# Performance work log

Measured on AMD Instinct MI355X. Metric: run time of the kernel, lower is better.

## Reference

```python
import jax, jax.numpy as jnp
import numpy as np

D_MODEL = 1024; D_STATE = 128; EXPAND = 2; HEADDIM = 64
D_INNER = EXPAND * D_MODEL; NHEADS = D_INNER // HEADDIM; PF = 2  # param_factor for complex
BATCH = 2; SEQ = 2048
DT_MIN = 0.001; DT_MAX = 0.1


def setup_inputs() -> dict:
    key = jax.random.key(0)
    k = jax.random.split(key, 10)
    u = jax.random.normal(k[0], (BATCH, SEQ, D_MODEL), jnp.float32)
    in_proj_w = jax.random.normal(k[1], (2 * D_INNER, D_MODEL), jnp.float32) * (D_MODEL ** -0.5)
    dt_projs_weight = jax.random.normal(k[2], (NHEADS, D_INNER), jnp.float32) * 0.02
    dt_projs_bias = (jax.random.uniform(k[3], (NHEADS,), jnp.float32)
                     * (np.log(DT_MAX) - np.log(DT_MIN)) + np.log(DT_MIN)).astype(jnp.float32)
    x_proj_w = jax.random.normal(k[4], (NHEADS * (1 + 2 * D_STATE * PF), D_INNER), jnp.float32) * (D_INNER ** -0.5)
    A = jnp.stack([-jax.random.uniform(k[5], (NHEADS, D_STATE), dtype=jnp.float32),
                   jax.random.normal(k[6], (NHEADS, D_STATE), jnp.float32) * 0.1], axis=-1)  # (H,N,2)
    D = jnp.ones((NHEADS,), jnp.float32)
    norm_B_w = jnp.ones((2 * D_STATE,), jnp.float32)
    norm_C_w = jnp.ones((2 * D_STATE,), jnp.float32)
    out_proj_w = jax.random.normal(k[7], (D_MODEL, D_INNER), jnp.float32) * (D_INNER ** -0.5)
    return {"u": u, "in_proj_w": in_proj_w, "dt_projs_weight": dt_projs_weight,
            "dt_projs_bias": dt_projs_bias, "x_proj_w": x_proj_w, "A": A, "D": D,
            "norm_B_w": norm_B_w, "norm_C_w": norm_C_w, "out_proj_w": out_proj_w}


def _rms_norm(x, w, eps=1e-6):
    return x * jax.lax.rsqrt(jnp.mean(x * x, axis=-1, keepdims=True) + eps) * w


def reference(u, in_proj_w, dt_projs_weight, dt_projs_bias, x_proj_w, A, D,
              norm_B_w, norm_C_w, out_proj_w):
    Bsz, L, _ = u.shape
    xz = u @ in_proj_w.T                        # (B,L,2*d_inner)
    x, z = jnp.split(xz, 2, axis=-1)
    x = jax.nn.silu(x)                          # (B,L,d_inner)
    dt = jax.nn.softplus(x @ dt_projs_weight.T + dt_projs_bias)  # (B,L,H)

    BCp = (x @ x_proj_w.T).reshape(Bsz, L, NHEADS, -1)
    BC = BCp[..., :2 * D_STATE * PF].reshape(Bsz, L, NHEADS, 2, D_STATE, PF)
    Bn = _rms_norm(BC[..., 0, :, :].reshape(Bsz, L, NHEADS, D_STATE * PF), norm_B_w)
    Cn = _rms_norm(BC[..., 1, :, :].reshape(Bsz, L, NHEADS, D_STATE * PF), norm_C_w)
    Bn = Bn.reshape(Bsz, L, NHEADS, D_STATE, PF)
    Cn = Cn.reshape(Bsz, L, NHEADS, D_STATE, PF)
    Bc = jax.lax.complex(Bn[..., 0], Bn[..., 1])  # (B,L,H,N) complex64
    Cc = jax.lax.complex(Cn[..., 0], Cn[..., 1])
    Ac = jax.lax.complex(A[..., 0], A[..., 1])    # (H,N) complex64

    xh = x.reshape(Bsz, L, NHEADS, HEADDIM)
    x_sum = xh.sum(axis=-1)                       # (B,L,H) -- kernel sums x_t over headdim
    zt = Ac[None, None] * (0.5 * dt)[..., None]   # (B,L,H,N) complex: A*dt/2
    den = 1.0 - zt
    abar = (1.0 + zt) / den                       # bilinear (Tustin) discretization
    u_in = Bc * ((dt * x_sum)[..., None] / den)   # Bbar * sum(x_t)

    def step(h, inp):
        a, b = inp
        h = a * h + b
        return h, h

    h0 = jnp.zeros((Bsz, NHEADS, D_STATE), jnp.complex64)
    _, hs = jax.lax.scan(step, h0, (jnp.swapaxes(abar, 0, 1), jnp.swapaxes(u_in, 0, 1)))
    hs = jnp.swapaxes(hs, 0, 1)                   # (B,L,H,N)
    y_red = jnp.real(Cc * hs).sum(axis=-1)        # (B,L,H), Re(C*h) reduced over state
    y = (xh * (y_red + D)[..., None]).reshape(Bsz, L, D_INNER)
    y = y * jax.nn.silu(z)
    return y @ out_proj_w.T
```

## Files before the change

kernel.cpp:

```cpp
#include <hip/hip_runtime.h>

#define BATCH   2
#define SEQ     2048
#define DMODEL  1024
#define DINNER  2048
#define NHEADS  32
#define HEADDIM 64
#define DSTATE  128
#define BLTOT   (BATCH * SEQ)
#define NCHUNK  32
#define CHUNK   64

#define OFF_UB   0ull
#define OFF_WXZ  8388608ull
#define OFF_WBC  16777216ull
#define OFF_WOUT 83886080ull
#define OFF_XB   88080384ull
#define OFF_YB   104857600ull
#define OFF_BC   121634816ull
#define OFF_SZ   255852544ull
#define OFF_DT   272629760ull
#define OFF_XS   273154048ull
#define OFF_YR   273678336ull
#define OFF_CA   274202624ull
#define OFF_CS   276299776ull
#define OFF_HI   278396928ull

typedef __attribute__((ext_vector_type(8))) short bf16x8;
typedef __attribute__((ext_vector_type(4))) float f32x4;

__device__ __forceinline__ float b2f(unsigned short u) {
    return __uint_as_float(((unsigned)u) << 16);
}
__device__ __forceinline__ unsigned short f2b(float f) {
    unsigned x = __float_as_uint(f);
    unsigned r = (x + 0x7fffu + ((x >> 16) & 1u)) >> 16;
    return (unsigned short)r;
}
__device__ __forceinline__ float silu_f(float v) {
    return v / (1.0f + __expf(-v));
}
__device__ __forceinline__ float softplus_f(float v) {
    return (v > 20.0f) ? v : log1pf(__expf(v));
}

__device__ __forceinline__ void gload_lds16(const void* g, void* l) {
    __builtin_amdgcn_global_load_lds(
        (const __attribute__((address_space(1))) unsigned int*)g,
        (__attribute__((address_space(3))) unsigned int*)l, 16, 0, 0);
}

__global__ __launch_bounds__(256) void conv_all_kernel(
    const float* __restrict__ u, const float* __restrict__ ipw,
    const float* __restrict__ opw, const float* __restrict__ xpw,
    unsigned short* __restrict__ u_b, unsigned short* __restrict__ w_xz,
    unsigned short* __restrict__ w_out, unsigned short* __restrict__ w_bc) {
    long idx = (long)blockIdx.x * 256 + threadIdx.x;
    if (idx >= 2621440L) {
        long e = (idx - 2621440L) * 4;
        long c = e >> 11, k = e & 2047;
        const float* s = xpw + ((c >> 9) * 513 + (c & 511)) * 2048 + k;
        float4 v = *(const float4*)s;
        ushort4 o = {f2b(v.x), f2b(v.y), f2b(v.z), f2b(v.w)};
        *(ushort4*)&w_bc[e] = o;
        return;
    }
    const float* src;
    unsigned short* dst;
    long i;
    if (idx < 1048576L)      { src = u;   dst = u_b;   i = idx; }
    else if (idx < 2097152L) { src = ipw; dst = w_xz;  i = idx - 1048576L; }
    else                     { src = opw; dst = w_out; i = idx - 2097152L; }
    float4 v = *(const float4*)&src[i * 4];
    ushort4 o = {f2b(v.x), f2b(v.y), f2b(v.z), f2b(v.w)};
    *(ushort4*)&dst[i * 4] = o;
}

template <int K, int MODE>
__global__ __launch_bounds__(256) void gemm_mfma(
    const unsigned short* __restrict__ A, const unsigned short* __restrict__ B,
    void* __restrict__ C0, void* __restrict__ C1, float* __restrict__ C2,
    int N) {
    __shared__ short ldsA[128 * 32];
    __shared__ short ldsB[128 * 32];
    int tid = threadIdx.x;
    int row0 = blockIdx.y * 128, col0 = blockIdx.x * 128;
    int lane = tid & 63, wave = tid >> 6;
    int wrow = (wave >> 1) * 64, wcol = (wave & 1) * 64;
    int m = lane & 15, quad = lane >> 4;

    f32x4 acc[4][4];
#pragma unroll
    for (int i = 0; i < 4; ++i)
#pragma unroll
        for (int j = 0; j < 4; ++j) acc[i][j] = (f32x4){0.f, 0.f, 0.f, 0.f};

    int r = tid >> 2, c8 = (tid & 3) * 8;
    const unsigned short* Ag = A + (size_t)(row0 + r) * K + c8;
    const unsigned short* Bg = B + (size_t)(col0 + r) * K + c8;
    short* la = ldsA + tid * 8;
    short* lb = ldsB + tid * 8;

    for (int k0 = 0; k0 < K; k0 += 32) {
        gload_lds16(Ag + k0, la);
        gload_lds16(Ag + (size_t)64 * K + k0, la + 2048);
        gload_lds16(Bg + k0, lb);
        gload_lds16(Bg + (size_t)64 * K + k0, lb + 2048);
        __syncthreads();
        bf16x8 af[4], bfr[4];
#pragma unroll
        for (int i = 0; i < 4; ++i)
            af[i] = *(const bf16x8*)&ldsA[(wrow + i * 16 + m) * 32 + quad * 8];
#pragma unroll
        for (int j = 0; j < 4; ++j)
            bfr[j] = *(const bf16x8*)&ldsB[(wcol + j * 16 + m) * 32 + quad * 8];
#pragma unroll
        for (int i = 0; i < 4; ++i)
#pragma unroll
            for (int j = 0; j < 4; ++j)
                acc[i][j] = __builtin_amdgcn_mfma_f32_16x16x32_bf16(
                    af[i], bfr[j], acc[i][j], 0, 0, 0);
        __syncthreads();
    }

    if (MODE == 1) {
        bool isx = (col0 < DINNER);
        if (isx) {
            int head = (col0 + wcol) >> 6;
            float ssum[4][4];
#pragma unroll
            for (int i = 0; i < 4; ++i)
#pragma unroll
                for (int reg = 0; reg < 4; ++reg) ssum[i][reg] = 0.f;
#pragma unroll
            for (int i = 0; i < 4; ++i)
#pragma unroll
                for (int reg = 0; reg < 4; ++reg) {
                    int row = row0 + wrow + i * 16 + quad * 4 + reg;
#pragma unroll
                    for (int j = 0; j < 4; ++j) {
                        int col = col0 + wcol + j * 16 + m;
                        float s = silu_f(acc[i][j][reg]);
                        ((unsigned short*)C0)[(size_t)row * DINNER + col] = f2b(s);
                        ssum[i][reg] += s;
                    }
                }
#pragma unroll
            for (int i = 0; i < 4; ++i)
#pragma unroll
                for (int reg = 0; reg < 4; ++reg) {
                    float s = ssum[i][reg];
                    s += __shfl_xor(s, 1);
                    s += __shfl_xor(s, 2);
                    s += __shfl_xor(s, 4);
                    s += __shfl_xor(s, 8);
                    if (m == 0) {
                        int row = row0 + wrow + i * 16 + quad * 4 + reg;
                        C2[(size_t)row * NHEADS + head] = s;
                    }
                }
        } else {
#pragma unroll
            for (int i = 0; i < 4; ++i)
#pragma unroll
                for (int reg = 0; reg < 4; ++reg) {
                    int row = row0 + wrow + i * 16 + quad * 4 + reg;
#pragma unroll
                    for (int j = 0; j < 4; ++j) {
                        int col = col0 + wcol + j * 16 + m - DINNER;
                        float s = silu_f(acc[i][j][reg]);
                        ((unsigned short*)C1)[(size_t)row * DINNER + col] = f2b(s);
                    }
                }
        }
    } else {
#pragma unroll
        for (int i = 0; i < 4; ++i)
#pragma unroll
            for (int reg = 0; reg < 4; ++reg) {
                int row = row0 + wrow + i * 16 + quad * 4 + reg;
#pragma unroll
                for (int j = 0; j < 4; ++j) {
                    int col = col0 + wcol + j * 16 + m;
                    float v = acc[i][j][reg];
                    if (MODE == 0)
                        ((float*)C0)[(size_t)row * N + col] = v;
                    else
                        ((unsigned short*)C0)[(size_t)row * N + col] = f2b(v);
                }
            }
    }
}

__global__ __launch_bounds__(256) void dt_kernel(
    const unsigned short* __restrict__ x, const float* __restrict__ dtw,
    const float* __restrict__ dtb, float* __restrict__ dt) {
    __shared__ float xs[16][132];
    __shared__ float ws[32][132];
    int r0 = blockIdx.x * 16;
    int t = threadIdx.x;
    int lrow = t >> 4, lc8 = (t & 15) * 8;
    int lh = t >> 3, lc16 = (t & 7) * 16;
    int row = t >> 4, h0 = t & 15;
    float acc0 = 0.f, acc1 = 0.f;

    for (int kc = 0; kc < DINNER; kc += 128) {
        ushort4 a = *(const ushort4*)&x[(size_t)(r0 + lrow) * DINNER + kc + lc8];
        ushort4 b = *(const ushort4*)&x[(size_t)(r0 + lrow) * DINNER + kc + lc8 + 4];
        xs[lrow][lc8 + 0] = b2f(a.x); xs[lrow][lc8 + 1] = b2f(a.y);
        xs[lrow][lc8 + 2] = b2f(a.z); xs[lrow][lc8 + 3] = b2f(a.w);
        xs[lrow][lc8 + 4] = b2f(b.x); xs[lrow][lc8 + 5] = b2f(b.y);
        xs[lrow][lc8 + 6] = b2f(b.z); xs[lrow][lc8 + 7] = b2f(b.w);
#pragma unroll
        for (int q = 0; q < 4; ++q) {
            float4 w = *(const float4*)&dtw[(size_t)lh * DINNER + kc + lc16 + q * 4];
            *(float4*)&ws[lh][lc16 + q * 4] = w;
        }
        __syncthreads();
#pragma unroll
        for (int k = 0; k < 128; k += 4) {
            float4 xv = *(const float4*)&xs[row][k];
            float4 w0 = *(const float4*)&ws[h0][k];
            float4 w1 = *(const float4*)&ws[h0 + 16][k];
            acc0 += xv.x * w0.x + xv.y * w0.y + xv.z * w0.z + xv.w * w0.w;
            acc1 += xv.x * w1.x + xv.y * w1.y + xv.z * w1.z + xv.w * w1.w;
        }
        __syncthreads();
    }
    dt[(size_t)(r0 + row) * NHEADS + h0]      = softplus_f(acc0 + dtb[h0]);
    dt[(size_t)(r0 + row) * NHEADS + h0 + 16] = softplus_f(acc1 + dtb[h0 + 16]);
}

__device__ __forceinline__ void coefs(
    float ar, float ai, float dtv, float xsv, float Br, float Bi,
    float& abr, float& abi, float& ur, float& ui) {
    float hd = 0.5f * dtv;
    float ztr = ar * hd, zti = ai * hd;
    float denr = 1.0f - ztr;
    float s2 = 1.0f / (denr * denr + zti * zti);
    float invr = denr * s2, invi = zti * s2;
    float opr = 1.0f + ztr;
    abr = opr * invr - zti * invi;
    abi = opr * invi + zti * invr;
    float coef = dtv * xsv;
    float cr = coef * invr, ci = coef * invi;
    ur = Br * cr - Bi * ci;
    ui = Br * ci + Bi * cr;
}

__global__ __launch_bounds__(64) void scan_pass1(
    const unsigned short* __restrict__ bc, const float* __restrict__ dt,
    const float* __restrict__ xsum, const float* __restrict__ A,
    const float* __restrict__ wB, float2* __restrict__ cA,
    float2* __restrict__ cS) {
    int blk = blockIdx.x;
    int bh = blk >> 5, c = blk & (NCHUNK - 1);
    int b = bh >> 5, h = bh & 31;
    int t = threadIdx.x;
    float4 av = *(const float4*)&A[(h * DSTATE + 2 * t) * 2];
    float4 wv = *(const float4*)&wB[4 * t];
    int l0 = c * CHUNK;
    const unsigned short* base = bc + ((size_t)(b * SEQ + l0)) * 16384 + h * 512;
    const float* dtp = dt + (b * SEQ + l0) * NHEADS + h;
    const float* xsp = xsum + (b * SEQ + l0) * NHEADS + h;

    float pr0 = 1.f, pi0 = 0.f, sr0 = 0.f, si0 = 0.f;
    float pr1 = 1.f, pi1 = 0.f, sr1 = 0.f, si1 = 0.f;
    for (int l = 0; l < CHUNK; ++l) {
        uint2 bw = *(const uint2*)&base[(size_t)l * 16384 + 4 * t];
        float Br0 = b2f((unsigned short)(bw.x & 0xffff));
        float Bi0 = b2f((unsigned short)(bw.x >> 16));
        float Br1 = b2f((unsigned short)(bw.y & 0xffff));
        float Bi1 = b2f((unsigned short)(bw.y >> 16));
        float ss = Br0 * Br0 + Bi0 * Bi0 + Br1 * Br1 + Bi1 * Bi1;
#pragma unroll
        for (int off = 1; off < 64; off <<= 1) ss += __shfl_xor(ss, off);
        float scale = rsqrtf(ss * (1.0f / 256.0f) + 1e-6f);
        Br0 *= scale * wv.x; Bi0 *= scale * wv.y;
        Br1 *= scale * wv.z; Bi1 *= scale * wv.w;
        float dtv = dtp[l * NHEADS], xsv = xsp[l * NHEADS];
        float abr, abi, ur, ui;
        coefs(av.x, av.y, dtv, xsv, Br0, Bi0, abr, abi, ur, ui);
        float ns = abr * sr0 - abi * si0 + ur;
        float nsi = abr * si0 + abi * sr0 + ui;
        sr0 = ns; si0 = nsi;
        float np = abr * pr0 - abi * pi0;
        float npi = abr * pi0 + abi * pr0;
        pr0 = np; pi0 = npi;
        coefs(av.z, av.w, dtv, xsv, Br1, Bi1, abr, abi, ur, ui);
        ns = abr * sr1 - abi * si1 + ur;
        nsi = abr * si1 + abi * sr1 + ui;
        sr1 = ns; si1 = nsi;
        np = abr * pr1 - abi * pi1;
        npi = abr * pi1 + abi * pr1;
        pr1 = np; pi1 = npi;
    }
    size_t idx = ((size_t)bh * NCHUNK + c) * DSTATE + 2 * t;
    *(float4*)&cA[idx] = (float4){pr0, pi0, pr1, pi1};
    *(float4*)&cS[idx] = (float4){sr0, si0, sr1, si1};
}

__global__ __launch_bounds__(128) void scan_fixup(
    const float2* __restrict__ cA, const float2* __restrict__ cS,
    float2* __restrict__ hin) {
    int bh = blockIdx.x;
    int n = threadIdx.x;
    float hr = 0.f, hi = 0.f;
    for (int c = 0; c < NCHUNK; ++c) {
        size_t idx = ((size_t)bh * NCHUNK + c) * DSTATE + n;
        hin[idx] = {hr, hi};
        float2 a = cA[idx];
        float2 s = cS[idx];
        float nhr = a.x * hr - a.y * hi + s.x;
        float nhi = a.x * hi + a.y * hr + s.y;
        hr = nhr; hi = nhi;
    }
}

__global__ __launch_bounds__(64) void scan_pass2(
    const unsigned short* __restrict__ bc, const float* __restrict__ dt,
    const float* __restrict__ xsum, const float* __restrict__ A,
    const float* __restrict__ wB, const float* __restrict__ wC,
    const float2* __restrict__ hin, float* __restrict__ yredp) {
    int blk = blockIdx.x;
    int bh = blk >> 5, c = blk & (NCHUNK - 1);
    int b = bh >> 5, h = bh & 31;
    int t = threadIdx.x;
    float4 av = *(const float4*)&A[(h * DSTATE + 2 * t) * 2];
    float4 wbv = *(const float4*)&wB[4 * t];
    float4 wcv = *(const float4*)&wC[4 * t];
    int l0 = c * CHUNK;
    const unsigned short* base = bc + ((size_t)(b * SEQ + l0)) * 16384 + h * 512;
    const float* dtp = dt + (b * SEQ + l0) * NHEADS + h;
    const float* xsp = xsum + (b * SEQ + l0) * NHEADS + h;
    float* yp = yredp + (size_t)(b * SEQ + l0) * NHEADS + h;

    float4 h0v = *(const float4*)&hin[((size_t)bh * NCHUNK + c) * DSTATE + 2 * t];
    float hr0 = h0v.x, hi0 = h0v.y, hr1 = h0v.z, hi1 = h0v.w;

    for (int l = 0; l < CHUNK; ++l) {
        uint2 bw = *(const uint2*)&base[(size_t)l * 16384 + 4 * t];
        uint2 cw = *(const uint2*)&base[(size_t)l * 16384 + 256 + 4 * t];
        float Br0 = b2f((unsigned short)(bw.x & 0xffff));
        float Bi0 = b2f((unsigned short)(bw.x >> 16));
        float Br1 = b2f((unsigned short)(bw.y & 0xffff));
        float Bi1 = b2f((unsigned short)(bw.y >> 16));
        float Cr0 = b2f((unsigned short)(cw.x & 0xffff));
        float Ci0 = b2f((unsigned short)(cw.x >> 16));
        float Cr1 = b2f((unsigned short)(cw.y & 0xffff));
        float Ci1 = b2f((unsigned short)(cw.y >> 16));
        float ssB = Br0 * Br0 + Bi0 * Bi0 + Br1 * Br1 + Bi1 * Bi1;
        float ssC = Cr0 * Cr0 + Ci0 * Ci0 + Cr1 * Cr1 + Ci1 * Ci1;
#pragma unroll
        for (int off = 1; off < 64; off <<= 1) {
            ssB += __shfl_xor(ssB, off);
            ssC += __shfl_xor(ssC, off);
        }
        float sB = rsqrtf(ssB * (1.0f / 256.0f) + 1e-6f);
        float sC = rsqrtf(ssC * (1.0f / 256.0f) + 1e-6f);
        Br0 *= sB * wbv.x; Bi0 *= sB * wbv.y;
        Br1 *= sB * wbv.z; Bi1 *= sB * wbv.w;
        Cr0 *= sC * wcv.x; Ci0 *= sC * wcv.y;
        Cr1 *= sC * wcv.z; Ci1 *= sC * wcv.w;
        float dtv = dtp[l * NHEADS], xsv = xsp[l * NHEADS];
        float abr, abi, ur, ui;
        coefs(av.x, av.y, dtv, xsv, Br0, Bi0, abr, abi, ur, ui);
        float nhr = abr * hr0 - abi * hi0 + ur;
        float nhi = abr * hi0 + abi * hr0 + ui;
        hr0 = nhr; hi0 = nhi;
        coefs(av.z, av.w, dtv, xsv, Br1, Bi1, abr, abi, ur, ui);
        nhr = abr * hr1 - abi * hi1 + ur;
        nhi = abr * hi1 + abi * hr1 + ui;
        hr1 = nhr; hi1 = nhi;
        float y = Cr0 * hr0 - Ci0 * hi0 + Cr1 * hr1 - Ci1 * hi1;
#pragma unroll
        for (int off = 1; off < 64; off <<= 1) y += __shfl_xor(y, off);
        if (t == 0) yp[(size_t)l * NHEADS] = y;
    }
}

__global__ __launch_bounds__(256) void yfuse_kernel(
    const unsigned short* __restrict__ x, const unsigned short* __restrict__ sz,
    const float* __restrict__ yredp, const float* __restrict__ Dv,
    unsigned short* __restrict__ y) {
    int i = (blockIdx.x * 256 + threadIdx.x) * 4;
    int r = i >> 11;
    int k = i & (DINNER - 1);
    int h = k >> 6;
    float yr = yredp[(size_t)r * NHEADS + h] + Dv[h];
    ushort4 xv = *(const ushort4*)&x[i];
    ushort4 zv = *(const ushort4*)&sz[i];
    ushort4 o = {f2b(b2f(xv.x) * yr * b2f(zv.x)),
                 f2b(b2f(xv.y) * yr * b2f(zv.y)),
                 f2b(b2f(xv.z) * yr * b2f(zv.z)),
                 f2b(b2f(xv.w) * yr * b2f(zv.w))};
    *(ushort4*)&y[i] = o;
}

extern "C" void kernel_launch(void* const* d_in, const int* in_sizes, int n_in,
                              void* d_out, int out_size, void* d_ws, size_t ws_size,
                              hipStream_t stream) {
    const float* u   = (const float*)d_in[0];
    const float* ipw = (const float*)d_in[1];
    const float* dtw = (const float*)d_in[2];
    const float* dtb = (const float*)d_in[3];
    const float* xpw = (const float*)d_in[4];
    const float* A   = (const float*)d_in[5];
    const float* Dv  = (const float*)d_in[6];
    const float* wB  = (const float*)d_in[7];
    const float* wC  = (const float*)d_in[8];
    const float* opw = (const float*)d_in[9];
    float* out = (float*)d_out;
    char* ws = (char*)d_ws;

    unsigned short* u_b   = (unsigned short*)(ws + OFF_UB);
    unsigned short* w_xz  = (unsigned short*)(ws + OFF_WXZ);
    unsigned short* w_bc  = (unsigned short*)(ws + OFF_WBC);
    unsigned short* w_out = (unsigned short*)(ws + OFF_WOUT);
    unsigned short* x_b   = (unsigned short*)(ws + OFF_XB);
    unsigned short* y_b   = (unsigned short*)(ws + OFF_YB);
    unsigned short* bc    = (unsigned short*)(ws + OFF_BC);
    unsigned short* sz    = (unsigned short*)(ws + OFF_SZ);
    float* dt    = (float*)(ws + OFF_DT);
    float* xsum  = (float*)(ws + OFF_XS);
    float* yredp = (float*)(ws + OFF_YR);
    float2* cA   = (float2*)(ws + OFF_CA);
    float2* cS   = (float2*)(ws + OFF_CS);
    float2* hin  = (float2*)(ws + OFF_HI);

    conv_all_kernel<<<43008, 256, 0, stream>>>(u, ipw, opw, xpw,
                                               u_b, w_xz, w_out, w_bc);

    gemm_mfma<1024, 1><<<dim3(32, 32), 256, 0, stream>>>(
        u_b, w_xz, x_b, sz, xsum, 4096);
    dt_kernel<<<BLTOT / 16, 256, 0, stream>>>(x_b, dtw, dtb, dt);
    gemm_mfma<2048, 2><<<dim3(128, 32), 256, 0, stream>>>(
        x_b, w_bc, bc, nullptr, nullptr, 16384);

    scan_pass1<<<BATCH * NHEADS * NCHUNK, 64, 0, stream>>>(
        bc, dt, xsum, A, wB, cA, cS);
    scan_fixup<<<BATCH * NHEADS, 128, 0, stream>>>(cA, cS, hin);
    scan_pass2<<<BATCH * NHEADS * NCHUNK, 64, 0, stream>>>(
        bc, dt, xsum, A, wB, wC, hin, yredp);

    yfuse_kernel<<<BLTOT * DINNER / 4 / 256, 256, 0, stream>>>(
        x_b, sz, yredp, Dv, y_b);
    gemm_mfma<2048, 0><<<dim3(8, 32), 256, 0, stream>>>(
        y_b, w_out, out, nullptr, nullptr, 1024);
}
```

Baseline: 837.5 us.

## Fuse RMS sum-of-squares into BC GEMM epilogue and split-K the out projection

The BC projection GEMM epilogue now accumulates per-row, per-(head,B/C) sums of squares via shuffles and atomics into a small buffer. The scan passes read these instead of doing wave-wide shuffle reductions every timestep. The output GEMM is split four ways along K with atomicAdd into a pre-zeroed output, giving 1024 blocks instead of 256 to fill the GPU. This adds two memsets and float atomics, so output summation order becomes nondeterministic. The norms are now taken from fp32 accumulators rather than bf16-rounded values.

```diff
diff --git a/kernel.cpp b/kernel.cpp
--- a/kernel.cpp
+++ b/kernel.cpp
@@ -25,6 +25,7 @@
 #define OFF_CA   274202624ull
 #define OFF_CS   276299776ull
 #define OFF_HI   278396928ull
+#define OFF_SS   280494080ull
 
 typedef __attribute__((ext_vector_type(8))) short bf16x8;
 typedef __attribute__((ext_vector_type(4))) float f32x4;
@@ -76,11 +77,11 @@
     *(ushort4*)&dst[i * 4] = o;
 }
 
-template <int K, int MODE>
-__global__ __launch_bounds__(256) void gemm_mfma(
+template <int KTOT, int KLEN, int MODE>
+__device__ __forceinline__ void gemm_body(
     const unsigned short* __restrict__ A, const unsigned short* __restrict__ B,
     void* __restrict__ C0, void* __restrict__ C1, float* __restrict__ C2,
-    int N) {
+    float* __restrict__ ssbuf, int N, int koff) {
     __shared__ short ldsA[128 * 32];
     __shared__ short ldsB[128 * 32];
     int tid = threadIdx.x;
@@ -96,16 +97,16 @@
         for (int j = 0; j < 4; ++j) acc[i][j] = (f32x4){0.f, 0.f, 0.f, 0.f};
 
     int r = tid >> 2, c8 = (tid & 3) * 8;
-    const unsigned short* Ag = A + (size_t)(row0 + r) * K + c8;
-    const unsigned short* Bg = B + (size_t)(col0 + r) * K + c8;
+    const unsigned short* Ag = A + (size_t)(row0 + r) * KTOT + koff + c8;
+    const unsigned short* Bg = B + (size_t)(col0 + r) * KTOT + koff + c8;
     short* la = ldsA + tid * 8;
     short* lb = ldsB + tid * 8;
 
-    for (int k0 = 0; k0 < K; k0 += 32) {
+    for (int k0 = 0; k0 < KLEN; k0 += 32) {
         gload_lds16(Ag + k0, la);
-        gload_lds16(Ag + (size_t)64 * K + k0, la + 2048);
+        gload_lds16(Ag + (size_t)64 * KTOT + k0, la + 2048);
         gload_lds16(Bg + k0, lb);
-        gload_lds16(Bg + (size_t)64 * K + k0, lb + 2048);
+        gload_lds16(Bg + (size_t)64 * KTOT + k0, lb + 2048);
         __syncthreads();
         bf16x8 af[4], bfr[4];
 #pragma unroll
@@ -173,7 +174,13 @@
                     }
                 }
         }
-    } else {
+    } else if (MODE == 2) {
+        int g = (col0 + wcol) >> 8;
+        float ssq[4][4];
+#pragma unroll
+        for (int i = 0; i < 4; ++i)
+#pragma unroll
+            for (int reg = 0; reg < 4; ++reg) ssq[i][reg] = 0.f;
 #pragma unroll
         for (int i = 0; i < 4; ++i)
 #pragma unroll
@@ -183,13 +190,55 @@
                 for (int j = 0; j < 4; ++j) {
                     int col = col0 + wcol + j * 16 + m;
                     float v = acc[i][j][reg];
-                    if (MODE == 0)
-                        ((float*)C0)[(size_t)row * N + col] = v;
-                    else
-                        ((unsigned short*)C0)[(size_t)row * N + col] = f2b(v);
+                    ((unsigned short*)C0)[(size_t)row * N + col] = f2b(v);
+                    ssq[i][reg] += v * v;
                 }
             }
-    }
+#pragma unroll
+        for (int i = 0; i < 4; ++i)
+#pragma unroll
+            for (int reg = 0; reg < 4; ++reg) {
+                float s = ssq[i][reg];
+                s += __shfl_xor(s, 1);
+                s += __shfl_xor(s, 2);
+                s += __shfl_xor(s, 4);
+                s += __shfl_xor(s, 8);
+                if (m == 0) {
+                    int row = row0 + wrow + i * 16 + quad * 4 + reg;
+                    atomicAdd(&ssbuf[(size_t)row * 64 + g], s);
+                }
+            }
+    } else {
+#pragma unroll
+        for (int i = 0; i < 4; ++i)
+#pragma unroll
+            for (int reg = 0; reg < 4; ++reg) {
+                int row = row0 + wrow + i * 16 + quad * 4 + reg;
+#pragma unroll
+                for (int j = 0; j < 4; ++j) {
+                    int col = col0 + wcol + j * 16 + m;
+                    atomicAdd(&((float*)C0)[(size_t)row * N + col],
+                              acc[i][j][reg]);
+                }
+            }
+    }
+}
+
+__global__ __launch_bounds__(256) void gemm_xz_kernel(
+    const unsigned short* __restrict__ A, const unsigned short* __restrict__ B,
+    void* C0, void* C1, float* C2) {
+    gemm_body<1024, 1024, 1>(A, B, C0, C1, C2, nullptr, 4096, 0);
+}
+__global__ __launch_bounds__(256) void gemm_bc_kernel(
+    const unsigned short* __restrict__ A, const unsigned short* __restrict__ B,
+    void* C0, float* ssbuf) {
+    gemm_body<2048, 2048, 2>(A, B, C0, nullptr, nullptr, ssbuf, 16384, 0);
+}
+__global__ __launch_bounds__(256) void gemm_out_kernel(
+    const unsigned short* __restrict__ A, const unsigned short* __restrict__ B,
+    void* C0) {
+    gemm_body<2048, 512, 3>(A, B, C0, nullptr, nullptr, nullptr, 1024,
+                            blockIdx.z * 512);
 }
 
 __global__ __launch_bounds__(256) void dt_kernel(
@@ -251,8 +300,8 @@
 __global__ __launch_bounds__(64) void scan_pass1(
     const unsigned short* __restrict__ bc, const float* __restrict__ dt,
     const float* __restrict__ xsum, const float* __restrict__ A,
-    const float* __restrict__ wB, float2* __restrict__ cA,
-    float2* __restrict__ cS) {
+    const float* __restrict__ wB, const float* __restrict__ ssbuf,
+    float2* __restrict__ cA, float2* __restrict__ cS) {
     int blk = blockIdx.x;
     int bh = blk >> 5, c = blk & (NCHUNK - 1);
     int b = bh >> 5, h = bh & 31;
@@ -263,21 +312,17 @@
     const unsigned short* base = bc + ((size_t)(b * SEQ + l0)) * 16384 + h * 512;
     const float* dtp = dt + (b * SEQ + l0) * NHEADS + h;
     const float* xsp = xsum + (b * SEQ + l0) * NHEADS + h;
+    const float* ssp = ssbuf + (size_t)(b * SEQ + l0) * 64 + 2 * h;
 
     float pr0 = 1.f, pi0 = 0.f, sr0 = 0.f, si0 = 0.f;
     float pr1 = 1.f, pi1 = 0.f, sr1 = 0.f, si1 = 0.f;
     for (int l = 0; l < CHUNK; ++l) {
         uint2 bw = *(const uint2*)&base[(size_t)l * 16384 + 4 * t];
-        float Br0 = b2f((unsigned short)(bw.x & 0xffff));
-        float Bi0 = b2f((unsigned short)(bw.x >> 16));
-        float Br1 = b2f((unsigned short)(bw.y & 0xffff));
-        float Bi1 = b2f((unsigned short)(bw.y >> 16));
-        float ss = Br0 * Br0 + Bi0 * Bi0 + Br1 * Br1 + Bi1 * Bi1;
-#pragma unroll
-        for (int off = 1; off < 64; off <<= 1) ss += __shfl_xor(ss, off);
-        float scale = rsqrtf(ss * (1.0f / 256.0f) + 1e-6f);
-        Br0 *= scale * wv.x; Bi0 *= scale * wv.y;
-        Br1 *= scale * wv.z; Bi1 *= scale * wv.w;
+        float scale = rsqrtf(ssp[l * 64] * (1.0f / 256.0f) + 1e-6f);
+        float Br0 = b2f((unsigned short)(bw.x & 0xffff)) * scale * wv.x;
+        float Bi0 = b2f((unsigned short)(bw.x >> 16)) * scale * wv.y;
+        float Br1 = b2f((unsigned short)(bw.y & 0xffff)) * scale * wv.z;
+        float Bi1 = b2f((unsigned short)(bw.y >> 16)) * scale * wv.w;
         float dtv = dtp[l * NHEADS], xsv = xsp[l * NHEADS];
         float abr, abi, ur, ui;
         coefs(av.x, av.y, dtv, xsv, Br0, Bi0, abr, abi, ur, ui);
@@ -321,7 +366,8 @@
     const unsigned short* __restrict__ bc, const float* __restrict__ dt,
     const float* __restrict__ xsum, const float* __restrict__ A,
     const float* __restrict__ wB, const float* __restrict__ wC,
-    const float2* __restrict__ hin, float* __restrict__ yredp) {
+    const float* __restrict__ ssbuf, const float2* __restrict__ hin,
+    float* __restrict__ yredp) {
     int blk = blockIdx.x;
     int bh = blk >> 5, c = blk & (NCHUNK - 1);
     int b = bh >> 5, h = bh & 31;
@@ -333,6 +379,7 @@
     const unsigned short* base = bc + ((size_t)(b * SEQ + l0)) * 16384 + h * 512;
     const float* dtp = dt + (b * SEQ + l0) * NHEADS + h;
     const float* xsp = xsum + (b * SEQ + l0) * NHEADS + h;
+    const float* ssp = ssbuf + (size_t)(b * SEQ + l0) * 64 + 2 * h;
     float* yp = yredp + (size_t)(b * SEQ + l0) * NHEADS + h;
 
     float4 h0v = *(const float4*)&hin[((size_t)bh * NCHUNK + c) * DSTATE + 2 * t];
@@ -341,27 +388,16 @@
     for (int l = 0; l < CHUNK; ++l) {
         uint2 bw = *(const uint2*)&base[(size_t)l * 16384 + 4 * t];
         uint2 cw = *(const uint2*)&base[(size_t)l * 16384 + 256 + 4 * t];
-        float Br0 = b2f((unsigned short)(bw.x & 0xffff));
-        float Bi0 = b2f((unsigned short)(bw.x >> 16));
-        float Br1 = b2f((unsigned short)(bw.y & 0xffff));
-        float Bi1 = b2f((unsigned short)(bw.y >> 16));
-        float Cr0 = b2f((unsigned short)(cw.x & 0xffff));
-        float Ci0 = b2f((unsigned short)(cw.x >> 16));
-        float Cr1 = b2f((unsigned short)(cw.y & 0xffff));
-        float Ci1 = b2f((unsigned short)(cw.y >> 16));
-        float ssB = Br0 * Br0 + Bi0 * Bi0 + Br1 * Br1 + Bi1 * Bi1;
-        float ssC = Cr0 * Cr0 + Ci0 * Ci0 + Cr1 * Cr1 + Ci1 * Ci1;
-#pragma unroll
-        for (int off = 1; off < 64; off <<= 1) {
-            ssB += __shfl_xor(ssB, off);
-            ssC += __shfl_xor(ssC, off);
-        }
-        float sB = rsqrtf(ssB * (1.0f / 256.0f) + 1e-6f);
-        float sC = rsqrtf(ssC * (1.0f / 256.0f) + 1e-6f);
-        Br0 *= sB * wbv.x; Bi0 *= sB * wbv.y;
-        Br1 *= sB * wbv.z; Bi1 *= sB * wbv.w;
-        Cr0 *= sC * wcv.x; Ci0 *= sC * wcv.y;
-        Cr1 *= sC * wcv.z; Ci1 *= sC * wcv.w;
+        float sB = rsqrtf(ssp[l * 64 + 0] * (1.0f / 256.0f) + 1e-6f);
+        float sC = rsqrtf(ssp[l * 64 + 1] * (1.0f / 256.0f) + 1e-6f);
+        float Br0 = b2f((unsigned short)(bw.x & 0xffff)) * sB * wbv.x;
+        float Bi0 = b2f((unsigned short)(bw.x >> 16)) * sB * wbv.y;
+        float Br1 = b2f((unsigned short)(bw.y & 0xffff)) * sB * wbv.z;
+        float Bi1 = b2f((unsigned short)(bw.y >> 16)) * sB * wbv.w;
+        float Cr0 = b2f((unsigned short)(cw.x & 0xffff)) * sC * wcv.x;
+        float Ci0 = b2f((unsigned short)(cw.x >> 16)) * sC * wcv.y;
+        float Cr1 = b2f((unsigned short)(cw.y & 0xffff)) * sC * wcv.z;
+        float Ci1 = b2f((unsigned short)(cw.y >> 16)) * sC * wcv.w;
         float dtv = dtp[l * NHEADS], xsv = xsp[l * NHEADS];
         float abr, abi, ur, ui;
         coefs(av.x, av.y, dtv, xsv, Br0, Bi0, abr, abi, ur, ui);
@@ -427,24 +463,25 @@
     float2* cA   = (float2*)(ws + OFF_CA);
     float2* cS   = (float2*)(ws + OFF_CS);
     float2* hin  = (float2*)(ws + OFF_HI);
+    float* ssbuf = (float*)(ws + OFF_SS);
+
+    hipMemsetAsync(ssbuf, 0, (size_t)BLTOT * 64 * 4, stream);
+    hipMemsetAsync(out, 0, (size_t)BLTOT * DMODEL * 4, stream);
 
     conv_all_kernel<<<43008, 256, 0, stream>>>(u, ipw, opw, xpw,
                                                u_b, w_xz, w_out, w_bc);
 
-    gemm_mfma<1024, 1><<<dim3(32, 32), 256, 0, stream>>>(
-        u_b, w_xz, x_b, sz, xsum, 4096);
+    gemm_xz_kernel<<<dim3(32, 32), 256, 0, stream>>>(u_b, w_xz, x_b, sz, xsum);
     dt_kernel<<<BLTOT / 16, 256, 0, stream>>>(x_b, dtw, dtb, dt);
-    gemm_mfma<2048, 2><<<dim3(128, 32), 256, 0, stream>>>(
-        x_b, w_bc, bc, nullptr, nullptr, 16384);
+    gemm_bc_kernel<<<dim3(128, 32), 256, 0, stream>>>(x_b, w_bc, bc, ssbuf);
 
     scan_pass1<<<BATCH * NHEADS * NCHUNK, 64, 0, stream>>>(
-        bc, dt, xsum, A, wB, cA, cS);
+        bc, dt, xsum, A, wB, ssbuf, cA, cS);
     scan_fixup<<<BATCH * NHEADS, 128, 0, stream>>>(cA, cS, hin);
     scan_pass2<<<BATCH * NHEADS * NCHUNK, 64, 0, stream>>>(
-        bc, dt, xsum, A, wB, wC, hin, yredp);
+        bc, dt, xsum, A, wB, wC, ssbuf, hin, yredp);
 
     yfuse_kernel<<<BLTOT * DINNER / 4 / 256, 256, 0, stream>>>(
         x_b, sz, yredp, Dv, y_b);
-    gemm_mfma<2048, 0><<<dim3(8, 32), 256, 0, stream>>>(
-        y_b, w_out, out, nullptr, nullptr, 1024);
-}
+    gemm_out_kernel<<<dim3(8, 32, 4), 256, 0, stream>>>(y_b, w_out, out);
+}
```

New measurement: 884.6 us. +5.6%, slower.
